# Performance work log

Measured on AMD Instinct MI355X. Metric: run time of the kernel, lower is better.

## Reference

```python
import jax, jax.numpy as jnp
import numpy as np

B, N, C, H = 32, 197, 1024, 16
D = C // H          # head_dim = 64
FF = 4 * C          # mlp hidden = 4096
SCALE = D ** -0.5
LN_EPS = 1e-6


def fq(x, bits=8):
    """Symmetric per-tensor fake-quant with straight-through estimator."""
    qmax = 2.0 ** (bits - 1) - 1.0
    s = jnp.maximum(jnp.max(jnp.abs(x)) / qmax, 1e-8)
    xq = jnp.clip(jnp.round(x / s), -qmax, qmax) * s
    return x + jax.lax.stop_gradient(xq - x)


def layernorm(x, g, b):
    mu = jnp.mean(x, axis=-1, keepdims=True)
    var = jnp.mean(jnp.square(x - mu), axis=-1, keepdims=True)
    return (x - mu) * jax.lax.rsqrt(var + LN_EPS) * g + b


def qlinear(x, w, b):
    # QuantLinear: int8 fake-quant of activation and weight, then GEMM + bias
    return jnp.einsum('bnc,oc->bno', fq(x), fq(w)) + b


def int_softmax(attn):
    # QuantIntSoft: softmax on int8-quantized scores, output requantized to uint8 grid
    p = jax.nn.softmax(attn, axis=-1)
    pq = jnp.round(p * 255.0) / 255.0
    return p + jax.lax.stop_gradient(pq - p)


def setup_inputs() -> dict:
    key = jax.random.key(0)
    ks = jax.random.split(key, 8)
    f32 = jnp.float32
    return {
        'x': jax.random.normal(ks[0], (B, N, C), f32),
        'g1': jnp.ones((C,), f32), 'b1': jnp.zeros((C,), f32),
        'w_qkv': jax.random.normal(ks[1], (3 * C, C), f32) * 0.02,
        'b_qkv': jnp.zeros((3 * C,), f32),
        'w_proj': jax.random.normal(ks[2], (C, C), f32) * 0.02,
        'b_proj': jnp.zeros((C,), f32),
        'g2': jnp.ones((C,), f32), 'b2': jnp.zeros((C,), f32),
        'w_fc1': jax.random.normal(ks[3], (FF, C), f32) * 0.02,
        'b_fc1': jnp.zeros((FF,), f32),
        'w_fc2': jax.random.normal(ks[4], (C, FF), f32) * 0.02,
        'b_fc2': jnp.zeros((C,), f32),
    }


def reference(x, g1, b1, w_qkv, b_qkv, w_proj, b_proj, g2, b2, w_fc1, b_fc1, w_fc2, b_fc2):
    # --- attention branch ---
    xn = layernorm(x, g1, b1)                       # QLayerNorm (norm1)
    qkv = qlinear(xn, w_qkv, b_qkv)                 # attn_qkv (QuantLinear)
    qkv = fq(qkv)                                   # attn_qkv_output (QAct)
    qkv = qkv.reshape(B, N, 3, H, D).transpose(2, 0, 3, 1, 4)  # [3,B,H,N,D]
    q, k, v = qkv[0], qkv[1], qkv[2]
    attn = jnp.einsum('bhnd,bhmd->bhnm', q, k) * SCALE
    attn = fq(attn)                                 # kv_act (QAct, layer-wise)
    attn = int_softmax(attn)                        # QuantIntSoft
    xa = jnp.einsum('bhnm,bhmd->bhnd', attn, v)
    xa = xa.transpose(0, 2, 1, 3).reshape(B, N, C)
    xa = qlinear(xa, w_proj, b_proj)                # attn_proj (QuantLinear)
    xa = fq(xa)                                     # sv_attn (QAct)
    x = x + xa                                      # drop_path is identity at eval
    x = fq(x)                                       # residual1 (QAct)
    # --- mlp branch ---
    xn = layernorm(x, g2, b2)                       # norm2
    h = qlinear(xn, w_fc1, b_fc1)                   # mlp_fc1
    h = fq(jax.nn.gelu(h))                          # mlp_act (QAct with GELU)
    h = qlinear(h, w_fc2, b_fc2)                    # mlp_fc2
    h = fq(h)                                       # mlp_act2 (QAct)
    x = x + h
    x = fq(x)                                       # residual2 (QAct)
    return x
```

## Files before the change

kernel.cpp:

```cpp
#include <hip/hip_runtime.h>

#define ROWS 6304
#define MPAD 6400
#define CDIM 1024
#define QKVD 3072
#define FFD  4096
#define NSEQ 197
#define NBH  512
#define NPREP (3072 + ROWS)

typedef __attribute__((ext_vector_type(8))) short bf16x8;
typedef __attribute__((ext_vector_type(4))) float f32x4;
typedef __attribute__((ext_vector_type(4))) int i32x4;

__device__ __forceinline__ float fqv(float v, float s) {
    float q = rintf(v / s);
    q = fminf(fmaxf(q, -127.0f), 127.0f);
    return q * s;
}
__device__ __forceinline__ float gelu_f(float x) {
    const float c = 0.7978845608028654f;
    float t = tanhf(c * (x + 0.044715f * x * x * x));
    return 0.5f * x * (1.0f + t);
}
__device__ __forceinline__ short bf16_of_small_int(float q) {
    return (short)(__float_as_uint(q) >> 16);
}
__device__ __forceinline__ short q_bf16(float v, float s) {
    return bf16_of_small_int(fminf(fmaxf(rintf(v / s), -127.f), 127.f));
}
__device__ __forceinline__ float blockReduceSum(float v, float* sred) {
    int lane = threadIdx.x & 63, w = threadIdx.x >> 6;
    #pragma unroll
    for (int o = 32; o > 0; o >>= 1) v += __shfl_down(v, o);
    __syncthreads();
    if (lane == 0) sred[w] = v;
    __syncthreads();
    return sred[0] + sred[1] + sred[2] + sred[3];
}
__device__ __forceinline__ float blockReduceMax(float v, float* sred) {
    int lane = threadIdx.x & 63, w = threadIdx.x >> 6;
    #pragma unroll
    for (int o = 32; o > 0; o >>= 1) v = fmaxf(v, __shfl_down(v, o));
    __syncthreads();
    if (lane == 0) sred[w] = v;
    __syncthreads();
    return fmaxf(fmaxf(sred[0], sred[1]), fmaxf(sred[2], sred[3]));
}
__device__ __forceinline__ float blockReduceMax8(float v, float* sred) {
    int lane = threadIdx.x & 63, w = threadIdx.x >> 6;
    #pragma unroll
    for (int o = 32; o > 0; o >>= 1) v = fmaxf(v, __shfl_down(v, o));
    __syncthreads();
    if (lane == 0) sred[w] = v;
    __syncthreads();
    float m = sred[0];
    #pragma unroll
    for (int i = 1; i < 8; i++) m = fmaxf(m, sred[i]);
    return m;
}
__device__ __forceinline__ float pmax256(const float* part, int n, float* sred) {
    float m = 0.f;
    for (int i = threadIdx.x; i < n; i += 256) m = fmaxf(m, part[i]);
    return blockReduceMax(m, sred);
}
__device__ __forceinline__ float scale_v(float amv) {
    return fmaxf(amv / 127.0f, 1e-8f);
}
__device__ __forceinline__ float scale_of(const float* am) {
    return fmaxf(am[0] / 127.0f, 1e-8f);
}

__global__ __launch_bounds__(256) void prep_a_kernel(
    const float* __restrict__ w0, const float* __restrict__ w1,
    const float* __restrict__ w2, const float* __restrict__ w3,
    const float* __restrict__ x, const float* __restrict__ g1,
    const float* __restrict__ b1, float* __restrict__ part) {
    __shared__ float sred[4];
    int b = blockIdx.x, tid = threadIdx.x;
    if (b < 3072) {
        const float4* p; int base, nb;
        if (b < 768)       { p = (const float4*)w0; base = b;        nb = 768;  }
        else if (b < 1024) { p = (const float4*)w1; base = b - 768;  nb = 256;  }
        else if (b < 2048) { p = (const float4*)w2; base = b - 1024; nb = 1024; }
        else               { p = (const float4*)w3; base = b - 2048; nb = 1024; }
        float m = 0.f;
        #pragma unroll
        for (int it = 0; it < 4; it++) {
            float4 v = p[(long long)it * nb * 256 + (long long)base * 256 + tid];
            m = fmaxf(m, fmaxf(fmaxf(fabsf(v.x), fabsf(v.y)), fmaxf(fabsf(v.z), fabsf(v.w))));
        }
        m = blockReduceMax(m, sred);
        if (tid == 0) part[b] = m;
    } else {
        int row = b - 3072;
        float4 v = ((const float4*)(x + (size_t)row * CDIM))[tid];
        float sum = blockReduceSum(v.x + v.y + v.z + v.w, sred);
        float mu = sum * (1.0f / CDIM);
        float dx = v.x - mu, dy = v.y - mu, dz = v.z - mu, dw = v.w - mu;
        float var = blockReduceSum(dx * dx + dy * dy + dz * dz + dw * dw, sred) * (1.0f / CDIM);
        float rstd = rsqrtf(var + 1e-6f);
        float4 gv = ((const float4*)g1)[tid], bv = ((const float4*)b1)[tid];
        float ox = dx * rstd * gv.x + bv.x;
        float oy = dy * rstd * gv.y + bv.y;
        float oz = dz * rstd * gv.z + bv.z;
        float ow = dw * rstd * gv.w + bv.w;
        float m = fmaxf(fmaxf(fabsf(ox), fabsf(oy)), fmaxf(fabsf(oz), fabsf(ow)));
        m = blockReduceMax(m, sred);
        if (tid == 0) part[b] = m;
    }
}

__global__ __launch_bounds__(256) void reduce_am5_kernel(const float* __restrict__ part,
                                                         float* __restrict__ am) {
    __shared__ float sred[4];
    float m0 = 0.f, m1 = 0.f, m2 = 0.f, m3 = 0.f, m4 = 0.f;
    for (int i = threadIdx.x; i < NPREP; i += 256) {
        float v = part[i];
        if (i < 768) m0 = fmaxf(m0, v);
        else if (i < 1024) m1 = fmaxf(m1, v);
        else if (i < 2048) m2 = fmaxf(m2, v);
        else if (i < 3072) m3 = fmaxf(m3, v);
        else m4 = fmaxf(m4, v);
    }
    m0 = blockReduceMax(m0, sred);
    m1 = blockReduceMax(m1, sred);
    m2 = blockReduceMax(m2, sred);
    m3 = blockReduceMax(m3, sred);
    m4 = blockReduceMax(m4, sred);
    if (threadIdx.x == 0) { am[0] = m0; am[1] = m1; am[2] = m2; am[3] = m3; am[4] = m4; }
}

__global__ __launch_bounds__(256) void reduce_one_kernel(const float* __restrict__ part,
                                                         int n, float* __restrict__ amDst) {
    __shared__ float sred[4];
    float m = 0.f;
    for (int i = threadIdx.x; i < n; i += 256) m = fmaxf(m, part[i]);
    m = blockReduceMax(m, sred);
    if (threadIdx.x == 0) amDst[0] = m;
}

__global__ __launch_bounds__(256) void prep_b_kernel(
    const float* __restrict__ w0, signed char* __restrict__ d0,
    const float* __restrict__ w1, signed char* __restrict__ d1,
    const float* __restrict__ w2, signed char* __restrict__ d2,
    const float* __restrict__ w3, signed char* __restrict__ d3,
    const float* __restrict__ x, const float* __restrict__ g1,
    const float* __restrict__ b1, signed char* __restrict__ xnq,
    const float* __restrict__ am) {
    __shared__ float sred[4];
    int b = blockIdx.x, tid = threadIdx.x;
    if (b >= NPREP) {
        int row = ROWS + (b - NPREP);
        ((int*)xnq)[(size_t)row * (CDIM / 4) + tid] = 0;
        return;
    }
    if (b < 3072) {
        const float4* p; int* d; int base, nb; float s;
        if (b < 768)       { p = (const float4*)w0; d = (int*)d0; base = b;        nb = 768;  s = scale_of(am + 0); }
        else if (b < 1024) { p = (const float4*)w1; d = (int*)d1; base = b - 768;  nb = 256;  s = scale_of(am + 1); }
        else if (b < 2048) { p = (const float4*)w2; d = (int*)d2; base = b - 1024; nb = 1024; s = scale_of(am + 2); }
        else               { p = (const float4*)w3; d = (int*)d3; base = b - 2048; nb = 1024; s = scale_of(am + 3); }
        #pragma unroll
        for (int it = 0; it < 4; it++) {
            long long i = (long long)it * nb * 256 + (long long)base * 256 + tid;
            float4 v = p[i];
            int q0 = (int)fminf(fmaxf(rintf(v.x / s), -127.f), 127.f);
            int q1 = (int)fminf(fmaxf(rintf(v.y / s), -127.f), 127.f);
            int q2 = (int)fminf(fmaxf(rintf(v.z / s), -127.f), 127.f);
            int q3 = (int)fminf(fmaxf(rintf(v.w / s), -127.f), 127.f);
            d[i] = (q0 & 255) | ((q1 & 255) << 8) | ((q2 & 255) << 16) | (q3 << 24);
        }
    } else {
        int row = b - 3072;
        float4 v = ((const float4*)(x + (size_t)row * CDIM))[tid];
        float sum = blockReduceSum(v.x + v.y + v.z + v.w, sred);
        float mu = sum * (1.0f / CDIM);
        float dx = v.x - mu, dy = v.y - mu, dz = v.z - mu, dw = v.w - mu;
        float var = blockReduceSum(dx * dx + dy * dy + dz * dz + dw * dw, sred) * (1.0f / CDIM);
        float rstd = rsqrtf(var + 1e-6f);
        float4 gv = ((const float4*)g1)[tid], bv = ((const float4*)b1)[tid];
        float ox = dx * rstd * gv.x + bv.x;
        float oy = dy * rstd * gv.y + bv.y;
        float oz = dz * rstd * gv.z + bv.z;
        float ow = dw * rstd * gv.w + bv.w;
        float s = scale_of(am + 4);
        int q0 = (int)fminf(fmaxf(rintf(ox / s), -127.f), 127.f);
        int q1 = (int)fminf(fmaxf(rintf(oy / s), -127.f), 127.f);
        int q2 = (int)fminf(fmaxf(rintf(oz / s), -127.f), 127.f);
        int q3 = (int)fminf(fmaxf(rintf(ow / s), -127.f), 127.f);
        ((int*)xnq)[(size_t)row * (CDIM / 4) + tid] =
            (q0 & 255) | ((q1 & 255) << 8) | ((q2 & 255) << 16) | (q3 << 24);
    }
}

template <int MODE>
__global__ __launch_bounds__(256) void ln_kernel(
    const float* __restrict__ x, const float* __restrict__ g,
    const float* __restrict__ bb, signed char* __restrict__ dst,
    const float* __restrict__ partIn, int nIn,
    const float* __restrict__ amQ, float* __restrict__ part) {
    __shared__ float sred[4];
    int row = blockIdx.x;
    int t = threadIdx.x;
    float sIn = scale_v(pmax256(partIn, nIn, sred));
    float4 v = ((const float4*)(x + (size_t)row * CDIM))[t];
    v.x = fqv(v.x, sIn); v.y = fqv(v.y, sIn); v.z = fqv(v.z, sIn); v.w = fqv(v.w, sIn);
    float sum = blockReduceSum(v.x + v.y + v.z + v.w, sred);
    float mu = sum * (1.0f / CDIM);
    float dx = v.x - mu, dy = v.y - mu, dz = v.z - mu, dw = v.w - mu;
    float var = blockReduceSum(dx * dx + dy * dy + dz * dz + dw * dw, sred) * (1.0f / CDIM);
    float rstd = rsqrtf(var + 1e-6f);
    float4 gv = ((const float4*)g)[t], bv = ((const float4*)bb)[t];
    float ox = dx * rstd * gv.x + bv.x;
    float oy = dy * rstd * gv.y + bv.y;
    float oz = dz * rstd * gv.z + bv.z;
    float ow = dw * rstd * gv.w + bv.w;
    if (MODE == 0) {
        float m = fmaxf(fmaxf(fabsf(ox), fabsf(oy)), fmaxf(fabsf(oz), fabsf(ow)));
        m = blockReduceMax(m, sred);
        if (t == 0) part[row] = m;
    } else {
        float s = scale_of(amQ);
        int q0 = (int)fminf(fmaxf(rintf(ox / s), -127.f), 127.f);
        int q1 = (int)fminf(fmaxf(rintf(oy / s), -127.f), 127.f);
        int q2 = (int)fminf(fmaxf(rintf(oz / s), -127.f), 127.f);
        int q3 = (int)fminf(fmaxf(rintf(ow / s), -127.f), 127.f);
        ((int*)dst)[(size_t)row * (CDIM / 4) + t] =
            (q0 & 255) | ((q1 & 255) << 8) | ((q2 & 255) << 16) | (q3 << 24);
    }
}

__global__ __launch_bounds__(256) void fq_inplace_kernel(float* __restrict__ buf, long long n4,
                                                         const float* __restrict__ part, int np) {
    __shared__ float sred[4];
    float s = scale_v(pmax256(part, np, sred));
    float4* b4 = (float4*)buf;
    long long stride = (long long)gridDim.x * blockDim.x;
    for (long long i = (long long)blockIdx.x * blockDim.x + threadIdx.x; i < n4; i += stride) {
        float4 v = b4[i];
        v.x = fqv(v.x, s); v.y = fqv(v.y, s); v.z = fqv(v.z, s); v.w = fqv(v.w, s);
        b4[i] = v;
    }
}

__global__ __launch_bounds__(256) void addfq_kernel(const float* __restrict__ xin,
                                                    const float* __restrict__ partX, int nX,
                                                    float* __restrict__ buf, long long n4,
                                                    const float* __restrict__ partAm, int nAm,
                                                    float* __restrict__ partOut) {
    __shared__ float sred[4];
    float s = scale_v(pmax256(partAm, nAm, sred));
    float sx = partX ? scale_v(pmax256(partX, nX, sred)) : 0.f;
    const float4* x4 = (const float4*)xin;
    float4* b4 = (float4*)buf;
    float m = 0.f;
    long long stride = (long long)gridDim.x * blockDim.x;
    for (long long i = (long long)blockIdx.x * blockDim.x + threadIdx.x; i < n4; i += stride) {
        float4 v = x4[i];
        if (partX) { v.x = fqv(v.x, sx); v.y = fqv(v.y, sx); v.z = fqv(v.z, sx); v.w = fqv(v.w, sx); }
        float4 u = b4[i];
        u.x = v.x + fqv(u.x, s);
        u.y = v.y + fqv(u.y, s);
        u.z = v.z + fqv(u.z, s);
        u.w = v.w + fqv(u.w, s);
        b4[i] = u;
        m = fmaxf(m, fmaxf(fmaxf(fabsf(u.x), fabsf(u.y)), fmaxf(fabsf(u.z), fabsf(u.w))));
    }
    m = blockReduceMax(m, sred);
    if (threadIdx.x == 0) partOut[blockIdx.x] = m;
}

__global__ __launch_bounds__(256) void quant_i8_kernel(const float* __restrict__ src,
                                                       signed char* __restrict__ dst,
                                                       long long n4, long long npad4,
                                                       const float* __restrict__ part, int np) {
    __shared__ float sred[4];
    float s = scale_v(pmax256(part, np, sred));
    long long stride = (long long)gridDim.x * blockDim.x;
    for (long long i = (long long)blockIdx.x * blockDim.x + threadIdx.x; i < npad4; i += stride) {
        float4 v = make_float4(0.f, 0.f, 0.f, 0.f);
        if (i < n4) v = ((const float4*)src)[i];
        int q0 = (int)fminf(fmaxf(rintf(v.x / s), -127.f), 127.f);
        int q1 = (int)fminf(fmaxf(rintf(v.y / s), -127.f), 127.f);
        int q2 = (int)fminf(fmaxf(rintf(v.z / s), -127.f), 127.f);
        int q3 = (int)fminf(fmaxf(rintf(v.w / s), -127.f), 127.f);
        ((int*)dst)[i] = (q0 & 255) | ((q1 & 255) << 8) | ((q2 & 255) << 16) | (q3 << 24);
    }
}

__global__ __launch_bounds__(256) void qv_kernel(const float* __restrict__ qkvF,
                                                 short* __restrict__ qkvq,
                                                 short* __restrict__ vtq,
                                                 const float* __restrict__ part5, int np5) {
    __shared__ short T[NSEQ * 65];
    __shared__ float sred[4];
    float s = scale_v(pmax256(part5, np5, sred));
    int b = blockIdx.x, tid = threadIdx.x;
    if (b < 2048) {
        const long long n4 = (long long)ROWS * 512;
        for (long long i = (long long)b * 256 + tid; i < n4; i += (long long)2048 * 256) {
            long long row = i >> 9;
            int c4 = (int)(i & 511);
            float4 v = ((const float4*)(qkvF + row * QKVD))[c4];
            short4 o;
            o.x = q_bf16(v.x, s); o.y = q_bf16(v.y, s);
            o.z = q_bf16(v.z, s); o.w = q_bf16(v.w, s);
            ((short4*)(qkvq + row * QKVD))[c4] = o;
        }
    } else {
        int z = b - 2048, bb = z >> 4, hh = z & 15;
        const float* vb = qkvF + (size_t)bb * NSEQ * QKVD + 2048 + hh * 64;
        for (int c = tid; c < NSEQ * 16; c += 256) {
            int m = c >> 4, p = c & 15;
            float4 v = ((const float4*)(vb + (size_t)m * QKVD))[p];
            T[m * 65 + p * 4 + 0] = q_bf16(v.x, s);
            T[m * 65 + p * 4 + 1] = q_bf16(v.y, s);
            T[m * 65 + p * 4 + 2] = q_bf16(v.z, s);
            T[m * 65 + p * 4 + 3] = q_bf16(v.w, s);
        }
        __syncthreads();
        short* obase = vtq + (size_t)z * 64 * 256;
        for (int c = tid; c < 64 * 32; c += 256) {
            int d = c >> 5, sl = c & 31;
            int sp = sl ^ (d & 7);
            bf16x8 o;
            #pragma unroll
            for (int jj = 0; jj < 8; jj++) {
                int m = sl * 8 + jj;
                o[jj] = (m < NSEQ) ? T[m * 65 + d] : (short)0;
            }
            *(bf16x8*)&obase[d * 256 + sp * 8] = o;
        }
    }
}

#define GLL(gp, lp) __builtin_amdgcn_global_load_lds( \
    (const __attribute__((address_space(1))) void*)(gp), \
    (__attribute__((address_space(3))) void*)(lp), 16, 0, 0)

__global__ __launch_bounds__(256, 2) void attn_amax_kernel(
    const short* __restrict__ qkvq,
    const float* __restrict__ part5, int np5, float* __restrict__ part) {
    __shared__ __align__(16) short Qs[256 * 32];
    __shared__ __align__(16) short Ks[64 * 32];
    __shared__ float sred[4];
    const int tid = threadIdx.x, lane = tid & 63, wave = tid >> 6;
    const int z = blockIdx.z, b = z >> 4, hh = z & 15;
    const int n0 = blockIdx.x * 64;
    const float s5 = scale_v(pmax256(part5, np5, sred));
    const float sc = s5 * s5 * 0.125f;
    const short* qbase = qkvq + (size_t)b * NSEQ * QKVD + hh * 64;
    const short* kbase = qbase + 1024;

    f32x4 acc[4][4] = {};
    const int piece = (tid & 3) * 8;
    const short* srcA[4];
    #pragma unroll
    for (int i = 0; i < 4; i++) {
        int row = i * 64 + (tid >> 2);
        srcA[i] = qbase + (size_t)min(row, NSEQ - 1) * QKVD + piece;
    }
    const short* srcB = kbase + (size_t)min(n0 + (tid >> 2), NSEQ - 1) * QKVD + piece;
    const int lr = lane & 15;
    const int koff = (lane >> 4) * 8;

    for (int k0 = 0; k0 < 64; k0 += 32) {
        __syncthreads();
        #pragma unroll
        for (int i = 0; i < 4; i++) GLL(srcA[i] + k0, Qs + i * 2048 + wave * 512);
        GLL(srcB + k0, Ks + wave * 512);
        __syncthreads();

        bf16x8 a[4], bfr[4];
        #pragma unroll
        for (int i = 0; i < 4; i++)
            a[i] = *(const bf16x8*)&Qs[(wave * 64 + i * 16 + lr) * 32 + koff];
        #pragma unroll
        for (int j = 0; j < 4; j++)
            bfr[j] = *(const bf16x8*)&Ks[(j * 16 + lr) * 32 + koff];
        #pragma unroll
        for (int i = 0; i < 4; i++)
            #pragma unroll
            for (int j = 0; j < 4; j++)
                acc[i][j] = __builtin_amdgcn_mfma_f32_16x16x32_bf16(a[i], bfr[j], acc[i][j], 0, 0, 0);
    }

    const int cr = (lane >> 4) * 4;
    const int cc = lane & 15;
    float mloc = 0.f;
    #pragma unroll
    for (int i = 0; i < 4; i++) {
        #pragma unroll
        for (int j = 0; j < 4; j++) {
            int gn = n0 + j * 16 + cc;
            #pragma unroll
            for (int r = 0; r < 4; r++) {
                int gm = wave * 64 + i * 16 + cr + r;
                if (gm < NSEQ && gn < NSEQ)
                    mloc = fmaxf(mloc, fabsf(acc[i][j][r] * sc));
            }
        }
    }
    mloc = blockReduceMax(mloc, sred);
    if (tid == 0) part[z * 4 + blockIdx.x] = mloc;
}

__global__ __launch_bounds__(256, 2) void attn_fused_kernel(
    const short* __restrict__ qkvq, const short* __restrict__ vtq,
    float* __restrict__ xa,
    const float* __restrict__ part5, int np5,
    const float* __restrict__ part6, int np6,
    float* __restrict__ part) {
    __shared__ __align__(16) short Qs[64 * 64];
    __shared__ __align__(16) short UN[64 * 256];
    __shared__ __align__(16) short Vs[64 * 256];
    __shared__ float sred[4];
    const int tid = threadIdx.x, lane = tid & 63, wave = tid >> 6;
    const int z = blockIdx.z, b = z >> 4, hh = z & 15, rb = blockIdx.x;
    const float s5 = scale_v(pmax256(part5, np5, sred));
    const float s6 = scale_v(pmax256(part6, np6, sred));
    const float sc = s5 * s5 * 0.125f;
    const short* qbase = qkvq + (size_t)b * NSEQ * QKVD + hh * 64;
    const short* kbase = qbase + 1024;

    #pragma unroll
    for (int i = 0; i < 2; i++) {
        int c = tid + 256 * i;
        int r = c >> 3, sl = c & 7;
        int gr = min(rb * 64 + r, NSEQ - 1);
        GLL(qbase + (size_t)gr * QKVD + ((sl ^ (r & 7)) * 8), Qs + c * 8);
    }
    #pragma unroll
    for (int i = 0; i < 7; i++) {
        int c = tid + 256 * i;
        int n = c >> 3, sl = c & 7;
        int gn = min(n, NSEQ - 1);
        GLL(kbase + (size_t)gn * QKVD + ((sl ^ (n & 7)) * 8), UN + c * 8);
    }
    {
        const short* vsrc = vtq + (size_t)z * 64 * 256;
        #pragma unroll
        for (int i = 0; i < 8; i++) {
            int c = tid + 256 * i;
            GLL(vsrc + c * 8, Vs + c * 8);
        }
    }
    __syncthreads();

    const int lr = lane & 15, klane = lane >> 4;
    f32x4 acc[14];
    #pragma unroll
    for (int cb = 0; cb < 14; cb++) acc[cb] = (f32x4){0.f, 0.f, 0.f, 0.f};
    #pragma unroll
    for (int ks = 0; ks < 2; ks++) {
        int r = wave * 16 + lr;
        bf16x8 aq = *(const bf16x8*)&Qs[r * 64 + (((ks * 4 + klane) ^ (r & 7)) * 8)];
        #pragma unroll
        for (int cb = 0; cb < 14; cb++) {
            int n = cb * 16 + lr;
            bf16x8 bk = *(const bf16x8*)&UN[n * 64 + (((ks * 4 + klane) ^ (n & 7)) * 8)];
            acc[cb] = __builtin_amdgcn_mfma_f32_16x16x32_bf16(aq, bk, acc[cb], 0, 0, 0);
        }
    }
    __syncthreads();

    #pragma unroll
    for (int reg = 0; reg < 4; reg++) {
        int rloc = wave * 16 + klane * 4 + reg;
        float v[14], mx = -3.0e38f;
        #pragma unroll
        for (int cb = 0; cb < 14; cb++) {
            int col = cb * 16 + lr;
            float q = fqv(acc[cb][reg] * sc, s6);
            v[cb] = (col < NSEQ) ? q : -3.0e38f;
            mx = fmaxf(mx, v[cb]);
        }
        #pragma unroll
        for (int o = 8; o > 0; o >>= 1) mx = fmaxf(mx, __shfl_xor(mx, o));
        float e[14], sum = 0.f;
        #pragma unroll
        for (int cb = 0; cb < 14; cb++) {
            int col = cb * 16 + lr;
            e[cb] = (col < NSEQ) ? expf(v[cb] - mx) : 0.f;
            sum += e[cb];
        }
        #pragma unroll
        for (int o = 8; o > 0; o >>= 1) sum += __shfl_xor(sum, o);
        #pragma unroll
        for (int cb = 0; cb < 14; cb++) {
            int col = cb * 16 + lr;
            float plvl = (col < NSEQ) ? rintf(e[cb] / sum * 255.0f) : 0.f;
            UN[rloc * 256 + (((col >> 3) ^ (rloc & 7)) * 8) + (col & 7)] = bf16_of_small_int(plvl);
        }
    }
    __syncthreads();

    f32x4 acc2[4];
    #pragma unroll
    for (int j = 0; j < 4; j++) acc2[j] = (f32x4){0.f, 0.f, 0.f, 0.f};
    #pragma unroll
    for (int ks = 0; ks < 7; ks++) {
        int r = wave * 16 + lr;
        bf16x8 ap = *(const bf16x8*)&UN[r * 256 + (((ks * 4 + klane) ^ (r & 7)) * 8)];
        #pragma unroll
        for (int j = 0; j < 4; j++) {
            int d = j * 16 + lr;
            bf16x8 bv = *(const bf16x8*)&Vs[d * 256 + (((ks * 4 + klane) ^ (d & 7)) * 8)];
            acc2[j] = __builtin_amdgcn_mfma_f32_16x16x32_bf16(ap, bv, acc2[j], 0, 0, 0);
        }
    }
    const float sc2 = s5 * (1.0f / 255.0f);
    float mloc = 0.f;
    #pragma unroll
    for (int j = 0; j < 4; j++) {
        int d = j * 16 + lr;
        #pragma unroll
        for (int r = 0; r < 4; r++) {
            int grow = rb * 64 + wave * 16 + klane * 4 + r;
            if (grow < NSEQ) {
                float vv = acc2[j][r] * sc2;
                xa[((size_t)b * NSEQ + grow) * CDIM + hh * 64 + d] = vv;
                mloc = fmaxf(mloc, fabsf(vv));
            }
        }
    }
    mloc = blockReduceMax(mloc, sred);
    if (tid == 0) part[z * 4 + rb] = mloc;
}

template <int EPI>
__global__ __launch_bounds__(256, 4) void mfma_gemmS_kernel(
    const signed char* __restrict__ Aq, const signed char* __restrict__ Bq,
    const float* __restrict__ bias, float* __restrict__ C,
    int M, int N, int K, int NBX,
    const float* __restrict__ partA, int nA,
    const float* __restrict__ amB, float* __restrict__ partOut) {
    __shared__ __align__(16) signed char As[2][64 * 64];
    __shared__ __align__(16) signed char Bs[2][128 * 64];
    __shared__ float sred[4];
    const int tid = threadIdx.x;
    const int lane = tid & 63;
    const int wave = tid >> 6;
    const int wg = (blockIdx.x & 7) * ((int)gridDim.x >> 3) + ((int)blockIdx.x >> 3);
    const int n0 = (wg % NBX) * 128;
    const int m0 = (wg / NBX) * 64;
    const int wm = (wave >> 1) * 32;
    const int wn = (wave & 1) * 64;

    i32x4 acc[2][4] = {};

    const signed char* gA;
    {
        int row = tid >> 2;
        int gsl = ((tid & 3) ^ (row & 3)) * 16;
        gA = Aq + (size_t)(m0 + row) * K + gsl;
    }
    const signed char* gB[2];
    #pragma unroll
    for (int i = 0; i < 2; i++) {
        int s = tid + 256 * i;
        int row = s >> 2;
        int gsl = ((s & 3) ^ (row & 3)) * 16;
        gB[i] = Bq + (size_t)(n0 + row) * K + gsl;
    }
    const int lr = lane & 15;
    const int klane = lane >> 4;
    int offA[2], offB[4];
    #pragma unroll
    for (int i = 0; i < 2; i++) {
        int ra = wm + i * 16 + lr;
        offA[i] = ra * 64 + ((klane ^ (ra & 3)) * 16);
    }
    #pragma unroll
    for (int j = 0; j < 4; j++) {
        int rb = wn + j * 16 + lr;
        offB[j] = rb * 64 + ((klane ^ (rb & 3)) * 16);
    }

#define STAGES(buf, kk) do { \
    GLL(gA + (kk),    &As[buf][wave * 1024]); \
    GLL(gB[0] + (kk), &Bs[buf][wave * 1024]); \
    GLL(gB[1] + (kk), &Bs[buf][wave * 1024 + 4096]); \
} while (0)

#define COMPUTES(buf) do { \
    i32x4 a[2], b[4]; \
    _Pragma("unroll") \
    for (int i = 0; i < 2; i++) a[i] = *(const i32x4*)&As[buf][offA[i]]; \
    _Pragma("unroll") \
    for (int j = 0; j < 4; j++) b[j] = *(const i32x4*)&Bs[buf][offB[j]]; \
    _Pragma("unroll") \
    for (int i = 0; i < 2; i++) \
        _Pragma("unroll") \
        for (int j = 0; j < 4; j++) \
            acc[i][j] = __builtin_amdgcn_mfma_i32_16x16x64_i8(a[i], b[j], acc[i][j], 0, 0, 0); \
} while (0)

    STAGES(0, 0);
    __syncthreads();
    int k0 = 0;
    for (; k0 + 128 < K; k0 += 128) {
        STAGES(1, k0 + 64);
        COMPUTES(0);
        __syncthreads();
        STAGES(0, k0 + 128);
        COMPUTES(1);
        __syncthreads();
    }
    STAGES(1, k0 + 64);
    COMPUTES(0);
    __syncthreads();
    COMPUTES(1);
#undef STAGES
#undef COMPUTES

    const float sAB = scale_v(pmax256(partA, nA, sred)) * scale_of(amB);
    const int cr = (lane >> 4) * 4;
    const int cc = lane & 15;
    float mloc = 0.f;
    #pragma unroll
    for (int i = 0; i < 2; i++) {
        #pragma unroll
        for (int j = 0; j < 4; j++) {
            int gn = n0 + wn + j * 16 + cc;
            float bv = bias[gn];
            #pragma unroll
            for (int r = 0; r < 4; r++) {
                int gm = m0 + wm + i * 16 + cr + r;
                if (gm >= M) continue;
                float v = (float)acc[i][j][r] * sAB + bv;
                if (EPI == 1) v = gelu_f(v);
                C[(size_t)gm * N + gn] = v;
                mloc = fmaxf(mloc, fabsf(v));
            }
        }
    }
    mloc = blockReduceMax(mloc, sred);
    if (tid == 0) partOut[blockIdx.x] = mloc;
}

template <int EPI>
__global__ __launch_bounds__(512, 4) void mfma_gemm8_kernel(
    const signed char* __restrict__ Aq, const signed char* __restrict__ Bq,
    const float* __restrict__ bias, float* __restrict__ C,
    int M, int N, int K, int NBX,
    const float* __restrict__ amA, const float* __restrict__ amB,
    float* __restrict__ partOut) {
    __shared__ __align__(16) signed char As[2][256 * 64];
    __shared__ __align__(16) signed char Bs[2][128 * 64];
    __shared__ float sred[8];
    const int tid = threadIdx.x;
    const int lane = tid & 63;
    const int wave = tid >> 6;
    const int wg = (blockIdx.x & 7) * ((int)gridDim.x >> 3) + ((int)blockIdx.x >> 3);
    const int n0 = (wg % NBX) * 128;
    const int m0 = (wg / NBX) * 256;
    const int wm = (wave >> 1) * 64;
    const int wn = (wave & 1) * 64;
    const float sAB = scale_of(amA) * scale_of(amB);

    i32x4 acc[4][4] = {};

    const signed char* gA[2];
    #pragma unroll
    for (int i = 0; i < 2; i++) {
        int s = tid + 512 * i;
        int row = s >> 2;
        int gsl = ((s & 3) ^ (row & 3)) * 16;
        gA[i] = Aq + (size_t)(m0 + row) * K + gsl;
    }
    const signed char* gB;
    {
        int row = tid >> 2;
        int gsl = ((tid & 3) ^ (row & 3)) * 16;
        gB = Bq + (size_t)(n0 + row) * K + gsl;
    }
    const int lr = lane & 15;
    const int klane = lane >> 4;
    int offA[4], offB[4];
    #pragma unroll
    for (int i = 0; i < 4; i++) {
        int ra = wm + i * 16 + lr;
        int rb = wn + i * 16 + lr;
        offA[i] = ra * 64 + ((klane ^ (ra & 3)) * 16);
        offB[i] = rb * 64 + ((klane ^ (rb & 3)) * 16);
    }

#define STAGE(buf, kk) do { \
    GLL(gA[0] + (kk), &As[buf][wave * 1024]); \
    GLL(gA[1] + (kk), &As[buf][wave * 1024 + 8192]); \
    GLL(gB + (kk),    &Bs[buf][wave * 1024]); \
} while (0)

#define COMPUTE(buf) do { \
    i32x4 a[4], b[4]; \
    _Pragma("unroll") \
    for (int i = 0; i < 4; i++) { \
        a[i] = *(const i32x4*)&As[buf][offA[i]]; \
        b[i] = *(const i32x4*)&Bs[buf][offB[i]]; \
    } \
    _Pragma("unroll") \
    for (int i = 0; i < 4; i++) \
        _Pragma("unroll") \
        for (int j = 0; j < 4; j++) \
            acc[i][j] = __builtin_amdgcn_mfma_i32_16x16x64_i8(a[i], b[j], acc[i][j], 0, 0, 0); \
} while (0)

    STAGE(0, 0);
    __syncthreads();
    int k0 = 0;
    for (; k0 + 128 < K; k0 += 128) {
        STAGE(1, k0 + 64);
        COMPUTE(0);
        __syncthreads();
        STAGE(0, k0 + 128);
        COMPUTE(1);
        __syncthreads();
    }
    STAGE(1, k0 + 64);
    COMPUTE(0);
    __syncthreads();
    COMPUTE(1);
#undef STAGE
#undef COMPUTE

    const int cr = (lane >> 4) * 4;
    const int cc = lane & 15;
    float mloc = 0.f;
    #pragma unroll
    for (int i = 0; i < 4; i++) {
        #pragma unroll
        for (int j = 0; j < 4; j++) {
            int gn = n0 + wn + j * 16 + cc;
            float bv = bias[gn];
            #pragma unroll
            for (int r = 0; r < 4; r++) {
                int gm = m0 + wm + i * 16 + cr + r;
                if (gm >= M) continue;
                float v = (float)acc[i][j][r] * sAB + bv;
                if (EPI == 1) v = gelu_f(v);
                C[(size_t)gm * N + gn] = v;
                mloc = fmaxf(mloc, fabsf(v));
            }
        }
    }
    mloc = blockReduceMax8(mloc, sred);
    if (tid == 0) partOut[blockIdx.x] = mloc;
}

extern "C" void kernel_launch(void* const* d_in, const int* in_sizes, int n_in,
                              void* d_out, int out_size, void* d_ws, size_t ws_size,
                              hipStream_t stream) {
    (void)in_sizes; (void)n_in; (void)out_size; (void)ws_size;
    const float* x      = (const float*)d_in[0];
    const float* g1     = (const float*)d_in[1];
    const float* b1     = (const float*)d_in[2];
    const float* w_qkv  = (const float*)d_in[3];
    const float* b_qkv  = (const float*)d_in[4];
    const float* w_proj = (const float*)d_in[5];
    const float* b_proj = (const float*)d_in[6];
    const float* g2     = (const float*)d_in[7];
    const float* b2     = (const float*)d_in[8];
    const float* w_fc1  = (const float*)d_in[9];
    const float* b_fc1  = (const float*)d_in[10];
    const float* w_fc2  = (const float*)d_in[11];
    const float* b_fc2  = (const float*)d_in[12];
    float* out = (float*)d_out;
    float* ws  = (float*)d_ws;

    float* am       = ws;
    float* partP    = ws + 64;
    float* p_qkv    = partP + 16384;
    float* p_s      = p_qkv + 1024;
    float* p_xa     = p_s + 2048;
    float* p_proj   = p_xa + 2048;
    float* p_y      = p_proj + 1024;
    float* p_ln     = p_y + 2048;
    float* p_fc1    = p_ln + 6400;
    float* p_fc2    = p_fc1 + 1024;
    float* p_r2     = p_fc2 + 1024;
    signed char* wq_qkv  = (signed char*)(p_r2 + 2048);
    signed char* wq_proj = wq_qkv + (size_t)QKVD * CDIM;
    signed char* wq_fc1  = wq_proj + (size_t)CDIM * CDIM;
    signed char* wq_fc2  = wq_fc1 + (size_t)FFD * CDIM;
    signed char* xnq     = wq_fc2 + (size_t)CDIM * FFD;
    float* y             = (float*)(xnq + (size_t)MPAD * CDIM);
    short* qkvq          = (short*)(y + (size_t)ROWS * CDIM);
    float* qkvF          = (float*)(qkvq + (size_t)ROWS * QKVD);
    short* vtq           = (short*)y;
    float* h             = (float*)qkvq;
    signed char* hq      = (signed char*)(h + (size_t)ROWS * FFD);
    float* xa = out;

    prep_a_kernel<<<NPREP, 256, 0, stream>>>(w_qkv, w_proj, w_fc1, w_fc2, x, g1, b1, partP);
    reduce_am5_kernel<<<1, 256, 0, stream>>>(partP, am);
    prep_b_kernel<<<NPREP + (MPAD - ROWS), 256, 0, stream>>>(
        w_qkv, wq_qkv, w_proj, wq_proj, w_fc1, wq_fc1, w_fc2, wq_fc2,
        x, g1, b1, xnq, am);

    mfma_gemm8_kernel<0><<<600, 512, 0, stream>>>(
        xnq, wq_qkv, b_qkv, qkvF, ROWS, QKVD, CDIM, QKVD / 128, am + 4, am + 0, p_qkv);
    qv_kernel<<<2048 + NBH, 256, 0, stream>>>(qkvF, qkvq, vtq, p_qkv, 600);

    attn_amax_kernel<<<dim3(4, 1, NBH), 256, 0, stream>>>(qkvq, p_qkv, 600, p_s);
    attn_fused_kernel<<<dim3(4, 1, NBH), 256, 0, stream>>>(
        qkvq, vtq, xa, p_qkv, 600, p_s, NBH * 4, p_xa);

    quant_i8_kernel<<<2048, 256, 0, stream>>>(xa, xnq,
        (long long)ROWS * CDIM / 4, (long long)MPAD * CDIM / 4, p_xa, NBH * 4);
    mfma_gemmS_kernel<0><<<800, 256, 0, stream>>>(
        xnq, wq_proj, b_proj, y, ROWS, CDIM, CDIM, CDIM / 128, p_xa, NBH * 4, am + 1, p_proj);

    addfq_kernel<<<2048, 256, 0, stream>>>(x, nullptr, 0, y, (long long)ROWS * CDIM / 4,
                                           p_proj, 800, p_y);

    ln_kernel<0><<<ROWS, 256, 0, stream>>>(y, g2, b2, nullptr, p_y, 2048, nullptr, p_ln);
    reduce_one_kernel<<<1, 256, 0, stream>>>(p_ln, ROWS, am + 10);
    ln_kernel<1><<<ROWS, 256, 0, stream>>>(y, g2, b2, xnq, p_y, 2048, am + 10, nullptr);

    mfma_gemm8_kernel<1><<<800, 512, 0, stream>>>(
        xnq, wq_fc1, b_fc1, h, ROWS, FFD, CDIM, FFD / 128, am + 10, am + 2, p_fc1);
    quant_i8_kernel<<<4096, 256, 0, stream>>>(h, hq,
        (long long)ROWS * FFD / 4, (long long)MPAD * FFD / 4, p_fc1, 800);

    mfma_gemmS_kernel<0><<<800, 256, 0, stream>>>(
        hq, wq_fc2, b_fc2, out, ROWS, CDIM, FFD, CDIM / 128, p_fc1, 800, am + 3, p_fc2);

    addfq_kernel<<<2048, 256, 0, stream>>>(y, p_y, 2048, out, (long long)ROWS * CDIM / 4,
                                           p_fc2, 800, p_r2);
    fq_inplace_kernel<<<2048, 256, 0, stream>>>(out, (long long)ROWS * CDIM / 4, p_r2, 2048);
}
```

Measured before the change: 450.3 us.

## Prefetch two K-stages ahead with explicit vmcnt waits in int8 GEMMs

Both int8 MFMA GEMM main loops now issue loads for two 64-wide K tiles up front. Each iteration waits only for the older tile via s_waitcnt vmcnt(3) instead of a full __syncthreads drain, then refills the freed buffer two stages ahead. The aim is to keep global-to-LDS loads in flight while MFMAs run, hiding memory latency. The hand-counted vmcnt depends on each stage issuing exactly three loads and on the compiler not reordering them. If that count is wrong, LDS reads could race with incoming data.

```diff
diff --git a/kernel.cpp b/kernel.cpp
--- a/kernel.cpp
+++ b/kernel.cpp
@@ -597,21 +597,20 @@
             acc[i][j] = __builtin_amdgcn_mfma_i32_16x16x64_i8(a[i], b[j], acc[i][j], 0, 0, 0); \
 } while (0)
 
+    asm volatile("s_waitcnt vmcnt(0)" ::: "memory");
     STAGES(0, 0);
-    __syncthreads();
-    int k0 = 0;
-    for (; k0 + 128 < K; k0 += 128) {
-        STAGES(1, k0 + 64);
-        COMPUTES(0);
-        __syncthreads();
-        STAGES(0, k0 + 128);
-        COMPUTES(1);
-        __syncthreads();
-    }
-    STAGES(1, k0 + 64);
-    COMPUTES(0);
-    __syncthreads();
-    COMPUTES(1);
+    STAGES(1, 64);
+    const int NK = K >> 6;
+    for (int t = 0; t < NK; ++t) {
+        if (t + 1 < NK) { asm volatile("s_waitcnt vmcnt(3)" ::: "memory"); }
+        else            { asm volatile("s_waitcnt vmcnt(0)" ::: "memory"); }
+        __builtin_amdgcn_sched_barrier(0);
+        __builtin_amdgcn_s_barrier();
+        COMPUTES(t & 1);
+        __builtin_amdgcn_s_barrier();
+        if (t + 2 < NK) STAGES(t & 1, (t + 2) << 6);
+    }
+    __builtin_amdgcn_sched_barrier(0);
 #undef STAGES
 #undef COMPUTES
 
@@ -707,21 +706,20 @@
             acc[i][j] = __builtin_amdgcn_mfma_i32_16x16x64_i8(a[i], b[j], acc[i][j], 0, 0, 0); \
 } while (0)
 
+    asm volatile("s_waitcnt vmcnt(0)" ::: "memory");
     STAGE(0, 0);
-    __syncthreads();
-    int k0 = 0;
-    for (; k0 + 128 < K; k0 += 128) {
-        STAGE(1, k0 + 64);
-        COMPUTE(0);
-        __syncthreads();
-        STAGE(0, k0 + 128);
-        COMPUTE(1);
-        __syncthreads();
-    }
-    STAGE(1, k0 + 64);
-    COMPUTE(0);
-    __syncthreads();
-    COMPUTE(1);
+    STAGE(1, 64);
+    const int NK = K >> 6;
+    for (int t = 0; t < NK; ++t) {
+        if (t + 1 < NK) { asm volatile("s_waitcnt vmcnt(3)" ::: "memory"); }
+        else            { asm volatile("s_waitcnt vmcnt(0)" ::: "memory"); }
+        __builtin_amdgcn_sched_barrier(0);
+        __builtin_amdgcn_s_barrier();
+        COMPUTE(t & 1);
+        __builtin_amdgcn_s_barrier();
+        if (t + 2 < NK) STAGE(t & 1, (t + 2) << 6);
+    }
+    __builtin_amdgcn_sched_barrier(0);
 #undef STAGE
 #undef COMPUTE
 
```

After: 445.9 us. Within noise of the previous version (-1.0%).
